# Performance work log

Hardware: AMD Instinct MI355X
Metric: run time of the kernel (lower is better)

Reference implementation:

```python
import jax, jax.numpy as jnp
import numpy as np
from jax import lax

SOS_TOKEN = 2  # prev_output initialized to [[2]] in the original module


def setup_inputs() -> dict:
    key = jax.random.key(0)
    ks = jax.random.split(key, 8)
    V, E, H, S = 32000, 512, 1024, 128
    return {
        "encoder_hn": jax.random.normal(ks[0], (1, 1, H), jnp.float32),
        "encoder_cn": jax.random.normal(ks[1], (1, 1, H), jnp.float32),
        "encoder_hidden_states": jax.random.normal(ks[2], (S, H), jnp.float32),
        "emb": jax.random.normal(ks[3], (V, E), jnp.float32) * 0.02,
        "W_ih": jax.random.normal(ks[4], (4 * H, E), jnp.float32) * 0.05,
        "W_hh": jax.random.normal(ks[5], (4 * H, H), jnp.float32) * 0.05,
        "b_ih": jnp.zeros((4 * H,), jnp.float32),
        "b_hh": jnp.zeros((4 * H,), jnp.float32),
        "W_fc": jax.random.normal(ks[6], (V, 2 * H), jnp.float32) * 0.02,
        "b_fc": jnp.zeros((V,), jnp.float32),
        "cutoff": 100,
    }


def reference(encoder_hn, encoder_cn, encoder_hidden_states, emb,
              W_ih, W_hh, b_ih, b_hh, W_fc, b_fc, cutoff):
    # Greedy sequential decode: embed -> LSTM cell -> dot attention -> concat -> fc -> log_softmax
    enc = encoder_hidden_states  # (S, H)

    def step(carry, _):
        tok, h, c = carry                       # tok: int scalar, h/c: (H,)
        x = emb[tok]                            # (E,) embedding lookup
        gates = W_ih @ x + b_ih + W_hh @ h + b_hh   # (4H,) torch LSTM gate order i,f,g,o
        i, f, g, o = jnp.split(gates, 4)
        i = jax.nn.sigmoid(i)
        f = jax.nn.sigmoid(f)
        g = jnp.tanh(g)
        o = jax.nn.sigmoid(o)
        c2 = f * c + i * g
        h2 = o * jnp.tanh(c2)
        # dot attention over encoder states
        scores = jax.nn.softmax(enc @ h2)       # (S,) softmax over seq dim
        ctx = scores @ enc                      # (H,) == enc.T @ scores
        concat = jnp.concatenate([h2, ctx])     # (2H,)
        logp = jax.nn.log_softmax(W_fc @ concat + b_fc)  # (V,)
        tok2 = jnp.argmax(logp)
        return (tok2, h2, c2), (logp, tok2)

    init = (jnp.asarray(SOS_TOKEN, jnp.int32), encoder_hn[0, 0], encoder_cn[0, 0])
    _, (preds, indices) = lax.scan(step, init, xs=None, length=int(cutoff))
    return preds, indices  # (cutoff, V), (cutoff,)
```

## Files before the change

kernel.cpp:

```cpp
#include <hip/hip_runtime.h>
#include <hip/hip_bf16.h>
#include <math.h>

#define V 32000
#define E 512
#define H 1024
#define SQ 128
#define T 100
#define NB 256
#define NTI 256
#define NTA 512
#define NTB 512
#define GROWS 16
#define FROWS 125
#define NEG_BIG (-1e30f)

typedef unsigned int u32;
typedef unsigned long long u64;

struct WS {
  float gates[4*H];
  float h[H];
  float c[2][H];
  float logits[V];
  float pmax[NB];
  float psum[NB];
  u64   pkey[NB];
};

__device__ __forceinline__ float wave_sum(float v){
  #pragma unroll
  for (int m = 32; m; m >>= 1) v += __shfl_xor(v, m, 64);
  return v;
}

__device__ __forceinline__ float wave_max(float v){
  #pragma unroll
  for (int m = 32; m; m >>= 1) v = fmaxf(v, __shfl_xor(v, m, 64));
  return v;
}

__device__ __forceinline__ u64 wave_max_u64(u64 v){
  #pragma unroll
  for (int m = 32; m; m >>= 1){
    u64 o = __shfl_xor(v, m, 64);
    v = (o > v) ? o : v;
  }
  return v;
}

__device__ __forceinline__ float dot4(float4 w, const float* v){
  return w.x*v[0] + w.y*v[1] + w.z*v[2] + w.w*v[3];
}

__global__ void __launch_bounds__(NTI) k_init(const float* __restrict__ hn,
                                              const float* __restrict__ cn,
                                              WS* __restrict__ ws){
  int tid = threadIdx.x;
  for (int j = tid; j < H; j += NTI){
    ws->h[j]    = hn[j];
    ws->c[0][j] = cn[j];
  }
  ws->pmax[tid] = NEG_BIG;
  ws->psum[tid] = 0.f;
  ws->pkey[tid] = 0ull;
}

__global__ void __launch_bounds__(NTA) k_a(const float* __restrict__ emb,
                                           const float* __restrict__ W_ih,
                                           const float* __restrict__ W_hh,
                                           const float* __restrict__ b_ih,
                                           const float* __restrict__ b_hh,
                                           WS* __restrict__ ws,
                                           float* __restrict__ out,
                                           int t){
  __shared__ float bc_logZ;
  __shared__ int   bc_tok;
  int b = blockIdx.x, tid = threadIdx.x;
  int wv = tid >> 6, ln = tid & 63;
  int tok = 2;

  if (t > 0){
    if (wv == 0){
      float mb0 = ws->pmax[ln],       mb1 = ws->pmax[ln+64];
      float mb2 = ws->pmax[ln+128],   mb3 = ws->pmax[ln+192];
      float sb0 = ws->psum[ln],       sb1 = ws->psum[ln+64];
      float sb2 = ws->psum[ln+128],   sb3 = ws->psum[ln+192];
      u64   kb0 = ws->pkey[ln],       kb1 = ws->pkey[ln+64];
      u64   kb2 = ws->pkey[ln+128],   kb3 = ws->pkey[ln+192];
      float m = wave_max(fmaxf(fmaxf(mb0, mb1), fmaxf(mb2, mb3)));
      float S = sb0*expf(mb0 - m) + sb1*expf(mb1 - m)
              + sb2*expf(mb2 - m) + sb3*expf(mb3 - m);
      S = wave_sum(S);
      u64 ka = (kb0 > kb1) ? kb0 : kb1;
      u64 kc = (kb2 > kb3) ? kb2 : kb3;
      u64 key = wave_max_u64((ka > kc) ? ka : kc);
      if (ln == 0){
        bc_logZ = m + logf(fmaxf(S, 1e-30f));
        int tk = (int)(~(u32)key);
        if ((u32)tk >= (u32)V) tk = 2;
        bc_tok = tk;
      }
    }
    __syncthreads();
    float logZ = bc_logZ;
    tok = bc_tok;

    if (tid < FROWS){
      int row = b*FROWS + tid;
      out[(size_t)(t-1)*V + row] = ws->logits[row] - logZ;
    }
    if (b == 0 && tid == 0)
      out[(size_t)T*V + (t-1)] = (float)tok;
  }

  if (t < T){
    float xv[8], hv[16];
    {
      const float4* xp = (const float4*)(emb + (size_t)tok*E) + ln*2;
      float4 x0 = xp[0], x1 = xp[1];
      xv[0]=x0.x; xv[1]=x0.y; xv[2]=x0.z; xv[3]=x0.w;
      xv[4]=x1.x; xv[5]=x1.y; xv[6]=x1.z; xv[7]=x1.w;
      const float4* hp = (const float4*)(ws->h) + ln*4;
      float4 h0 = hp[0], h1 = hp[1], h2 = hp[2], h3 = hp[3];
      hv[0]=h0.x; hv[1]=h0.y; hv[2]=h0.z; hv[3]=h0.w;
      hv[4]=h1.x; hv[5]=h1.y; hv[6]=h1.z; hv[7]=h1.w;
      hv[8]=h2.x; hv[9]=h2.y; hv[10]=h2.z; hv[11]=h2.w;
      hv[12]=h3.x; hv[13]=h3.y; hv[14]=h3.z; hv[15]=h3.w;
    }
    int rl0 = wv*2;
    int row0 = b*GROWS + rl0, row1 = row0 + 1;
    const float4* ap0 = (const float4*)(W_ih + (size_t)row0*E) + ln*2;
    const float4* ap1 = (const float4*)(W_ih + (size_t)row1*E) + ln*2;
    const float4* wh0 = (const float4*)(W_hh + (size_t)row0*H) + ln*4;
    const float4* wh1 = (const float4*)(W_hh + (size_t)row1*H) + ln*4;
    float4 ia[2], ib[2], ha[4], hb[4];
    #pragma unroll
    for (int k = 0; k < 2; ++k) ia[k] = ap0[k];
    #pragma unroll
    for (int k = 0; k < 2; ++k) ib[k] = ap1[k];
    #pragma unroll
    for (int k = 0; k < 4; ++k) ha[k] = wh0[k];
    #pragma unroll
    for (int k = 0; k < 4; ++k) hb[k] = wh1[k];
    float acc0 = dot4(ia[0], xv) + dot4(ia[1], xv+4)
               + dot4(ha[0], hv) + dot4(ha[1], hv+4) + dot4(ha[2], hv+8) + dot4(ha[3], hv+12);
    float acc1 = dot4(ib[0], xv) + dot4(ib[1], xv+4)
               + dot4(hb[0], hv) + dot4(hb[1], hv+4) + dot4(hb[2], hv+8) + dot4(hb[3], hv+12);
    acc0 = wave_sum(acc0);
    acc1 = wave_sum(acc1);
    if (ln == 0){
      ws->gates[row0] = acc0 + b_ih[row0] + b_hh[row0];
      ws->gates[row1] = acc1 + b_ih[row1] + b_hh[row1];
    }
  }
}

__global__ void __launch_bounds__(NTB) k_b(const float* __restrict__ enc,
                                           const float* __restrict__ W_fc,
                                           const float* __restrict__ b_fc,
                                           WS* __restrict__ ws,
                                           int t){
  __shared__ float concat[2*H];
  __shared__ float sc[SQ];
  __shared__ float pw[SQ];
  __shared__ float lg[128];
  int b = blockIdx.x, tid = threadIdx.x;
  int wv = tid >> 6, ln = tid & 63;

  {
    float c2v[2], h2v[2];
    #pragma unroll
    for (int k = 0; k < 2; ++k){
      int j = tid + k*NTB;
      float gi = ws->gates[j];
      float gf = ws->gates[H + j];
      float gg = ws->gates[2*H + j];
      float go = ws->gates[3*H + j];
      float co = ws->c[t & 1][j];
      float si = 1.f/(1.f + expf(-gi));
      float sf = 1.f/(1.f + expf(-gf));
      float tg = tanhf(gg);
      float so = 1.f/(1.f + expf(-go));
      float cn = sf*co + si*tg;
      float hn = so*tanhf(cn);
      c2v[k] = cn; h2v[k] = hn;
      concat[j] = hn;
    }
    if (b == 0){
      #pragma unroll
      for (int k = 0; k < 2; ++k){
        int j = tid + k*NTB;
        ws->c[(t+1) & 1][j] = c2v[k];
        ws->h[j] = h2v[k];
      }
    }
  }
  __syncthreads();

  {
    float hv[16];
    #pragma unroll
    for (int k = 0; k < 16; ++k) hv[k] = concat[ln*16 + k];
    #pragma unroll
    for (int u = 0; u < 8; ++u){
      int s0 = wv*16 + u*2, s1 = s0 + 1;
      const float4* e0p = (const float4*)(enc + (size_t)s0*H) + ln*4;
      const float4* e1p = (const float4*)(enc + (size_t)s1*H) + ln*4;
      float4 e0[4], e1[4];
      #pragma unroll
      for (int k = 0; k < 4; ++k) e0[k] = e0p[k];
      #pragma unroll
      for (int k = 0; k < 4; ++k) e1[k] = e1p[k];
      float acc0 = dot4(e0[0], hv) + dot4(e0[1], hv+4) + dot4(e0[2], hv+8) + dot4(e0[3], hv+12);
      float acc1 = dot4(e1[0], hv) + dot4(e1[1], hv+4) + dot4(e1[2], hv+8) + dot4(e1[3], hv+12);
      acc0 = wave_sum(acc0);
      acc1 = wave_sum(acc1);
      if (ln == 0){ sc[s0] = acc0; sc[s1] = acc1; }
    }
  }
  __syncthreads();

  if (wv == 0){
    float v0 = sc[ln], v1 = sc[ln + 64];
    float m = wave_max(fmaxf(v0, v1));
    float e0 = expf(v0 - m), e1 = expf(v1 - m);
    float S = wave_sum(e0 + e1);
    pw[ln]      = e0 / S;
    pw[ln + 64] = e1 / S;
  }
  __syncthreads();

  {
    float a0 = 0.f, a1 = 0.f;
    const float2* eb = (const float2*)enc + tid;
    #pragma unroll 8
    for (int s = 0; s < SQ; ++s){
      float2 e = eb[(size_t)s*(H/2)];
      float w = pw[s];
      a0 += w*e.x; a1 += w*e.y;
    }
    concat[H + tid*2 + 0] = a0;
    concat[H + tid*2 + 1] = a1;
  }
  __syncthreads();

  {
    float cv[32];
    #pragma unroll
    for (int k = 0; k < 8; ++k)
      #pragma unroll
      for (int m = 0; m < 4; ++m)
        cv[k*4 + m] = concat[k*256 + ln*4 + m];

    #pragma unroll
    for (int it = 0; it < 4; ++it){
      int l = wv*4 + it*32;
      int c0 = l,     c1 = l+1, c2 = l+2, c3 = l+3;
      if (c1 > FROWS-1) c1 = FROWS-1;
      if (c2 > FROWS-1) c2 = FROWS-1;
      if (c3 > FROWS-1) c3 = FROWS-1;
      const float4* p0 = (const float4*)(W_fc + (size_t)(b*FROWS + c0)*2048) + ln;
      const float4* p1 = (const float4*)(W_fc + (size_t)(b*FROWS + c1)*2048) + ln;
      const float4* p2 = (const float4*)(W_fc + (size_t)(b*FROWS + c2)*2048) + ln;
      const float4* p3 = (const float4*)(W_fc + (size_t)(b*FROWS + c3)*2048) + ln;
      float4 w0[8], w1[8], w2[8], w3[8];
      #pragma unroll
      for (int k = 0; k < 8; ++k) w0[k] = p0[(size_t)k*64];
      #pragma unroll
      for (int k = 0; k < 8; ++k) w1[k] = p1[(size_t)k*64];
      #pragma unroll
      for (int k = 0; k < 8; ++k) w2[k] = p2[(size_t)k*64];
      #pragma unroll
      for (int k = 0; k < 8; ++k) w3[k] = p3[(size_t)k*64];
      float a0 = 0.f, a1 = 0.f, a2 = 0.f, a3 = 0.f;
      #pragma unroll
      for (int k = 0; k < 8; ++k){
        a0 += dot4(w0[k], cv + k*4);
        a1 += dot4(w1[k], cv + k*4);
        a2 += dot4(w2[k], cv + k*4);
        a3 += dot4(w3[k], cv + k*4);
      }
      a0 = wave_sum(a0);
      a1 = wave_sum(a1);
      a2 = wave_sum(a2);
      a3 = wave_sum(a3);
      if (ln == 0){
        int row = b*FROWS + l;
        {            float x = a0 + b_fc[row];     ws->logits[row]   = x; lg[l]   = x; }
        if (l+1 < FROWS){ float x = a1 + b_fc[row+1]; ws->logits[row+1] = x; lg[l+1] = x; }
        if (l+2 < FROWS){ float x = a2 + b_fc[row+2]; ws->logits[row+2] = x; lg[l+2] = x; }
        if (l+3 < FROWS){ float x = a3 + b_fc[row+3]; ws->logits[row+3] = x; lg[l+3] = x; }
      }
    }
  }
  __syncthreads();

  if (wv == 0){
    float v0 = (ln < FROWS)      ? lg[ln]      : NEG_BIG;
    float v1 = (ln + 64 < FROWS) ? lg[ln + 64] : NEG_BIG;
    float mb = wave_max(fmaxf(v0, v1));
    float e  = expf(v0 - mb) + expf(v1 - mb);
    float sb = wave_sum(e);

    u64 k0 = 0ull, k1 = 0ull;
    if (ln < FROWS){
      u32 u = __float_as_uint(v0);
      u32 srt = (u >> 31) ? ~u : (u | 0x80000000u);
      k0 = ((u64)srt << 32) | (u32)(~(u32)(b*FROWS + ln));
    }
    if (ln + 64 < FROWS){
      u32 u = __float_as_uint(v1);
      u32 srt = (u >> 31) ? ~u : (u | 0x80000000u);
      k1 = ((u64)srt << 32) | (u32)(~(u32)(b*FROWS + ln + 64));
    }
    u64 key = wave_max_u64((k0 > k1) ? k0 : k1);

    if (ln == 0){
      ws->pmax[b] = mb;
      ws->psum[b] = sb;
      ws->pkey[b] = key;
    }
  }
}

extern "C" void kernel_launch(void* const* d_in, const int* in_sizes, int n_in,
                              void* d_out, int out_size, void* d_ws, size_t ws_size,
                              hipStream_t stream){
  const float* hn   = (const float*)d_in[0];
  const float* cn   = (const float*)d_in[1];
  const float* enc  = (const float*)d_in[2];
  const float* emb  = (const float*)d_in[3];
  const float* W_ih = (const float*)d_in[4];
  const float* W_hh = (const float*)d_in[5];
  const float* b_ih = (const float*)d_in[6];
  const float* b_hh = (const float*)d_in[7];
  const float* W_fc = (const float*)d_in[8];
  const float* b_fc = (const float*)d_in[9];
  float* out = (float*)d_out;
  WS* ws = (WS*)d_ws;
  if (ws_size < sizeof(WS)) return;

  k_init<<<1, NTI, 0, stream>>>(hn, cn, ws);
  for (int t = 0; t <= T; ++t){
    k_a<<<NB, NTA, 0, stream>>>(emb, W_ih, W_hh, b_ih, b_hh, ws, out, t);
    if (t < T) k_b<<<NB, NTB, 0, stream>>>(enc, W_fc, b_fc, ws, t);
  }
}
```

Baseline: 6.899 ms.

## Split attention into single-block kernel, removing redundant per-block attention in FC

```diff
diff --git a/kernel.cpp b/kernel.cpp
--- a/kernel.cpp
+++ b/kernel.cpp
@@ -10,7 +10,11 @@
 #define NB 256
 #define NTI 256
 #define NTA 512
-#define NTB 512
+#define NBB 500
+#define BROWS 64
+#define NTB 256
+#define NTC 1024
+#define NP 512
 #define GROWS 16
 #define FROWS 125
 #define NEG_BIG (-1e30f)
@@ -22,10 +26,11 @@
   float gates[4*H];
   float h[H];
   float c[2][H];
+  float concat[2*H];
   float logits[V];
-  float pmax[NB];
-  float psum[NB];
-  u64   pkey[NB];
+  float pmax[NP];
+  float psum[NP];
+  u64   pkey[NP];
 };
 
 __device__ __forceinline__ float wave_sum(float v){
@@ -61,9 +66,11 @@
     ws->h[j]    = hn[j];
     ws->c[0][j] = cn[j];
   }
-  ws->pmax[tid] = NEG_BIG;
-  ws->psum[tid] = 0.f;
-  ws->pkey[tid] = 0ull;
+  for (int i = tid; i < NP; i += NTI){
+    ws->pmax[i] = NEG_BIG;
+    ws->psum[i] = 0.f;
+    ws->pkey[i] = 0ull;
+  }
 }
 
 __global__ void __launch_bounds__(NTA) k_a(const float* __restrict__ emb,
@@ -82,19 +89,25 @@
 
   if (t > 0){
     if (wv == 0){
-      float mb0 = ws->pmax[ln],       mb1 = ws->pmax[ln+64];
-      float mb2 = ws->pmax[ln+128],   mb3 = ws->pmax[ln+192];
-      float sb0 = ws->psum[ln],       sb1 = ws->psum[ln+64];
-      float sb2 = ws->psum[ln+128],   sb3 = ws->psum[ln+192];
-      u64   kb0 = ws->pkey[ln],       kb1 = ws->pkey[ln+64];
-      u64   kb2 = ws->pkey[ln+128],   kb3 = ws->pkey[ln+192];
-      float m = wave_max(fmaxf(fmaxf(mb0, mb1), fmaxf(mb2, mb3)));
-      float S = sb0*expf(mb0 - m) + sb1*expf(mb1 - m)
-              + sb2*expf(mb2 - m) + sb3*expf(mb3 - m);
+      float mb[8], sb[8]; u64 kb[8];
+      #pragma unroll
+      for (int k = 0; k < 8; ++k){
+        mb[k] = ws->pmax[ln + k*64];
+        sb[k] = ws->psum[ln + k*64];
+        kb[k] = ws->pkey[ln + k*64];
+      }
+      float mx = mb[0];
+      #pragma unroll
+      for (int k = 1; k < 8; ++k) mx = fmaxf(mx, mb[k]);
+      float m = wave_max(mx);
+      float S = 0.f;
+      #pragma unroll
+      for (int k = 0; k < 8; ++k) S += sb[k] * expf(mb[k] - m);
       S = wave_sum(S);
-      u64 ka = (kb0 > kb1) ? kb0 : kb1;
-      u64 kc = (kb2 > kb3) ? kb2 : kb3;
-      u64 key = wave_max_u64((ka > kc) ? ka : kc);
+      u64 key = kb[0];
+      #pragma unroll
+      for (int k = 1; k < 8; ++k) key = (kb[k] > key) ? kb[k] : key;
+      key = wave_max_u64(key);
       if (ln == 0){
         bc_logZ = m + logf(fmaxf(S, 1e-30f));
         int tk = (int)(~(u32)key);
@@ -108,7 +121,8 @@
 
     if (tid < FROWS){
       int row = b*FROWS + tid;
-      out[(size_t)(t-1)*V + row] = ws->logits[row] - logZ;
+      __builtin_nontemporal_store(ws->logits[row] - logZ,
+                                  &out[(size_t)(t-1)*V + row]);
     }
     if (b == 0 && tid == 0)
       out[(size_t)T*V + (t-1)] = (float)tok;
@@ -156,55 +170,42 @@
   }
 }
 
-__global__ void __launch_bounds__(NTB) k_b(const float* __restrict__ enc,
-                                           const float* __restrict__ W_fc,
-                                           const float* __restrict__ b_fc,
+__global__ void __launch_bounds__(NTC) k_c(const float* __restrict__ enc,
                                            WS* __restrict__ ws,
                                            int t){
-  __shared__ float concat[2*H];
+  __shared__ float h2s[H];
   __shared__ float sc[SQ];
   __shared__ float pw[SQ];
-  __shared__ float lg[128];
-  int b = blockIdx.x, tid = threadIdx.x;
+  int tid = threadIdx.x;
   int wv = tid >> 6, ln = tid & 63;
 
   {
-    float c2v[2], h2v[2];
-    #pragma unroll
-    for (int k = 0; k < 2; ++k){
-      int j = tid + k*NTB;
-      float gi = ws->gates[j];
-      float gf = ws->gates[H + j];
-      float gg = ws->gates[2*H + j];
-      float go = ws->gates[3*H + j];
-      float co = ws->c[t & 1][j];
-      float si = 1.f/(1.f + expf(-gi));
-      float sf = 1.f/(1.f + expf(-gf));
-      float tg = tanhf(gg);
-      float so = 1.f/(1.f + expf(-go));
-      float cn = sf*co + si*tg;
-      float hn = so*tanhf(cn);
-      c2v[k] = cn; h2v[k] = hn;
-      concat[j] = hn;
-    }
-    if (b == 0){
-      #pragma unroll
-      for (int k = 0; k < 2; ++k){
-        int j = tid + k*NTB;
-        ws->c[(t+1) & 1][j] = c2v[k];
-        ws->h[j] = h2v[k];
-      }
-    }
+    int j = tid;
+    float gi = ws->gates[j];
+    float gf = ws->gates[H + j];
+    float gg = ws->gates[2*H + j];
+    float go = ws->gates[3*H + j];
+    float co = ws->c[t & 1][j];
+    float si = 1.f/(1.f + expf(-gi));
+    float sf = 1.f/(1.f + expf(-gf));
+    float tg = tanhf(gg);
+    float so = 1.f/(1.f + expf(-go));
+    float cn = sf*co + si*tg;
+    float hn = so*tanhf(cn);
+    ws->c[(t+1) & 1][j] = cn;
+    ws->h[j] = hn;
+    ws->concat[j] = hn;
+    h2s[j] = hn;
   }
   __syncthreads();
 
   {
     float hv[16];
     #pragma unroll
-    for (int k = 0; k < 16; ++k) hv[k] = concat[ln*16 + k];
-    #pragma unroll
-    for (int u = 0; u < 8; ++u){
-      int s0 = wv*16 + u*2, s1 = s0 + 1;
+    for (int k = 0; k < 16; ++k) hv[k] = h2s[ln*16 + k];
+    #pragma unroll
+    for (int u = 0; u < 4; ++u){
+      int s0 = wv*8 + u*2, s1 = s0 + 1;
       const float4* e0p = (const float4*)(enc + (size_t)s0*H) + ln*4;
       const float4* e1p = (const float4*)(enc + (size_t)s1*H) + ln*4;
       float4 e0[4], e1[4];
@@ -232,89 +233,83 @@
   __syncthreads();
 
   {
-    float a0 = 0.f, a1 = 0.f;
-    const float2* eb = (const float2*)enc + tid;
+    int col = tid;
+    float a = 0.f;
     #pragma unroll 8
-    for (int s = 0; s < SQ; ++s){
-      float2 e = eb[(size_t)s*(H/2)];
-      float w = pw[s];
-      a0 += w*e.x; a1 += w*e.y;
-    }
-    concat[H + tid*2 + 0] = a0;
-    concat[H + tid*2 + 1] = a1;
+    for (int s = 0; s < SQ; ++s)
+      a += pw[s] * enc[(size_t)s*H + col];
+    ws->concat[H + col] = a;
+  }
+}
+
+__global__ void __launch_bounds__(NTB) k_b(const float* __restrict__ W_fc,
+                                           const float* __restrict__ b_fc,
+                                           WS* __restrict__ ws){
+  __shared__ float lg[BROWS];
+  int b = blockIdx.x, tid = threadIdx.x;
+  int wv = tid >> 6, ln = tid & 63;
+
+  float cv[32];
+  {
+    const float4* cp = (const float4*)ws->concat + ln;
+    #pragma unroll
+    for (int k = 0; k < 8; ++k){
+      float4 v = cp[k*64];
+      cv[k*4+0] = v.x; cv[k*4+1] = v.y; cv[k*4+2] = v.z; cv[k*4+3] = v.w;
+    }
+  }
+
+  #pragma unroll
+  for (int it = 0; it < 4; ++it){
+    int l = wv*4 + it*16;
+    int row = b*BROWS + l;
+    const float4* p0 = (const float4*)(W_fc + (size_t)(row+0)*2048) + ln;
+    const float4* p1 = (const float4*)(W_fc + (size_t)(row+1)*2048) + ln;
+    const float4* p2 = (const float4*)(W_fc + (size_t)(row+2)*2048) + ln;
+    const float4* p3 = (const float4*)(W_fc + (size_t)(row+3)*2048) + ln;
+    float4 w0[8], w1[8], w2[8], w3[8];
+    #pragma unroll
+    for (int k = 0; k < 8; ++k) w0[k] = p0[(size_t)k*64];
+    #pragma unroll
+    for (int k = 0; k < 8; ++k) w1[k] = p1[(size_t)k*64];
+    #pragma unroll
+    for (int k = 0; k < 8; ++k) w2[k] = p2[(size_t)k*64];
+    #pragma unroll
+    for (int k = 0; k < 8; ++k) w3[k] = p3[(size_t)k*64];
+    float a0 = 0.f, a1 = 0.f, a2 = 0.f, a3 = 0.f;
+    #pragma unroll
+    for (int k = 0; k < 8; ++k){
+      a0 += dot4(w0[k], cv + k*4);
+      a1 += dot4(w1[k], cv + k*4);
+      a2 += dot4(w2[k], cv + k*4);
+      a3 += dot4(w3[k], cv + k*4);
+    }
+    a0 = wave_sum(a0);
+    a1 = wave_sum(a1);
+    a2 = wave_sum(a2);
+    a3 = wave_sum(a3);
+    if (ln == 0){
+      float x0 = a0 + b_fc[row+0];
+      float x1 = a1 + b_fc[row+1];
+      float x2 = a2 + b_fc[row+2];
+      float x3 = a3 + b_fc[row+3];
+      ws->logits[row+0] = x0; lg[l+0] = x0;
+      ws->logits[row+1] = x1; lg[l+1] = x1;
+      ws->logits[row+2] = x2; lg[l+2] = x2;
+      ws->logits[row+3] = x3; lg[l+3] = x3;
+    }
   }
   __syncthreads();
 
-  {
-    float cv[32];
-    #pragma unroll
-    for (int k = 0; k < 8; ++k)
-      #pragma unroll
-      for (int m = 0; m < 4; ++m)
-        cv[k*4 + m] = concat[k*256 + ln*4 + m];
-
-    #pragma unroll
-    for (int it = 0; it < 4; ++it){
-      int l = wv*4 + it*32;
-      int c0 = l,     c1 = l+1, c2 = l+2, c3 = l+3;
-      if (c1 > FROWS-1) c1 = FROWS-1;
-      if (c2 > FROWS-1) c2 = FROWS-1;
-      if (c3 > FROWS-1) c3 = FROWS-1;
-      const float4* p0 = (const float4*)(W_fc + (size_t)(b*FROWS + c0)*2048) + ln;
-      const float4* p1 = (const float4*)(W_fc + (size_t)(b*FROWS + c1)*2048) + ln;
-      const float4* p2 = (const float4*)(W_fc + (size_t)(b*FROWS + c2)*2048) + ln;
-      const float4* p3 = (const float4*)(W_fc + (size_t)(b*FROWS + c3)*2048) + ln;
-      float4 w0[8], w1[8], w2[8], w3[8];
-      #pragma unroll
-      for (int k = 0; k < 8; ++k) w0[k] = p0[(size_t)k*64];
-      #pragma unroll
-      for (int k = 0; k < 8; ++k) w1[k] = p1[(size_t)k*64];
-      #pragma unroll
-      for (int k = 0; k < 8; ++k) w2[k] = p2[(size_t)k*64];
-      #pragma unroll
-      for (int k = 0; k < 8; ++k) w3[k] = p3[(size_t)k*64];
-      float a0 = 0.f, a1 = 0.f, a2 = 0.f, a3 = 0.f;
-      #pragma unroll
-      for (int k = 0; k < 8; ++k){
-        a0 += dot4(w0[k], cv + k*4);
-        a1 += dot4(w1[k], cv + k*4);
-        a2 += dot4(w2[k], cv + k*4);
-        a3 += dot4(w3[k], cv + k*4);
-      }
-      a0 = wave_sum(a0);
-      a1 = wave_sum(a1);
-      a2 = wave_sum(a2);
-      a3 = wave_sum(a3);
-      if (ln == 0){
-        int row = b*FROWS + l;
-        {            float x = a0 + b_fc[row];     ws->logits[row]   = x; lg[l]   = x; }
-        if (l+1 < FROWS){ float x = a1 + b_fc[row+1]; ws->logits[row+1] = x; lg[l+1] = x; }
-        if (l+2 < FROWS){ float x = a2 + b_fc[row+2]; ws->logits[row+2] = x; lg[l+2] = x; }
-        if (l+3 < FROWS){ float x = a3 + b_fc[row+3]; ws->logits[row+3] = x; lg[l+3] = x; }
-      }
-    }
-  }
-  __syncthreads();
-
   if (wv == 0){
-    float v0 = (ln < FROWS)      ? lg[ln]      : NEG_BIG;
-    float v1 = (ln + 64 < FROWS) ? lg[ln + 64] : NEG_BIG;
-    float mb = wave_max(fmaxf(v0, v1));
-    float e  = expf(v0 - mb) + expf(v1 - mb);
-    float sb = wave_sum(e);
-
-    u64 k0 = 0ull, k1 = 0ull;
-    if (ln < FROWS){
-      u32 u = __float_as_uint(v0);
-      u32 srt = (u >> 31) ? ~u : (u | 0x80000000u);
-      k0 = ((u64)srt << 32) | (u32)(~(u32)(b*FROWS + ln));
-    }
-    if (ln + 64 < FROWS){
-      u32 u = __float_as_uint(v1);
-      u32 srt = (u >> 31) ? ~u : (u | 0x80000000u);
-      k1 = ((u64)srt << 32) | (u32)(~(u32)(b*FROWS + ln + 64));
-    }
-    u64 key = wave_max_u64((k0 > k1) ? k0 : k1);
+    float v = lg[ln];
+    float mb = wave_max(v);
+    float sb = wave_sum(expf(v - mb));
+
+    u32 u = __float_as_uint(v);
+    u32 srt = (u >> 31) ? ~u : (u | 0x80000000u);
+    u64 key = ((u64)srt << 32) | (u32)(~(u32)(b*BROWS + ln));
+    key = wave_max_u64(key);
 
     if (ln == 0){
       ws->pmax[b] = mb;
@@ -344,6 +339,9 @@
   k_init<<<1, NTI, 0, stream>>>(hn, cn, ws);
   for (int t = 0; t <= T; ++t){
     k_a<<<NB, NTA, 0, stream>>>(emb, W_ih, W_hh, b_ih, b_hh, ws, out, t);
-    if (t < T) k_b<<<NB, NTB, 0, stream>>>(enc, W_fc, b_fc, ws, t);
-  }
-}
+    if (t < T){
+      k_c<<<1,   NTC, 0, stream>>>(enc, ws, t);
+      k_b<<<NBB, NTB, 0, stream>>>(W_fc, b_fc, ws);
+    }
+  }
+}
```

New measurement: 7.578 ms. +9.8%, slower.

## Fuse decode loop into one persistent kernel with software grid barriers

Applied to the files above, without the earlier changes.

```diff
diff --git a/kernel.cpp b/kernel.cpp
--- a/kernel.cpp
+++ b/kernel.cpp
@@ -8,9 +8,11 @@
 #define SQ 128
 #define T 100
 #define NB 256
+#define NBLK 256
 #define NTI 256
 #define NTA 512
 #define NTB 512
+#define NT 512
 #define GROWS 16
 #define FROWS 125
 #define NEG_BIG (-1e30f)
@@ -26,6 +28,9 @@
   float pmax[NB];
   float psum[NB];
   u64   pkey[NB];
+  u32   pad[30];
+  u32   bar_cnt;
+  u32   bar_gen;
 };
 
 __device__ __forceinline__ float wave_sum(float v){
@@ -51,6 +56,24 @@
 
 __device__ __forceinline__ float dot4(float4 w, const float* v){
   return w.x*v[0] + w.y*v[1] + w.z*v[2] + w.w*v[3];
+}
+
+__device__ __forceinline__ void gsync(WS* ws){
+  __builtin_amdgcn_fence(__ATOMIC_RELEASE, "agent");
+  __syncthreads();
+  if (threadIdx.x == 0){
+    u32 g = __hip_atomic_load(&ws->bar_gen, __ATOMIC_RELAXED, __HIP_MEMORY_SCOPE_AGENT);
+    u32 a = __hip_atomic_fetch_add(&ws->bar_cnt, 1u, __ATOMIC_ACQ_REL, __HIP_MEMORY_SCOPE_AGENT);
+    if (a == (u32)(NBLK - 1)){
+      __hip_atomic_store(&ws->bar_cnt, 0u, __ATOMIC_RELAXED, __HIP_MEMORY_SCOPE_AGENT);
+      __hip_atomic_fetch_add(&ws->bar_gen, 1u, __ATOMIC_RELEASE, __HIP_MEMORY_SCOPE_AGENT);
+    } else {
+      while (__hip_atomic_load(&ws->bar_gen, __ATOMIC_RELAXED, __HIP_MEMORY_SCOPE_AGENT) == g)
+        __builtin_amdgcn_s_sleep(8);
+    }
+  }
+  __syncthreads();
+  __builtin_amdgcn_fence(__ATOMIC_ACQUIRE, "agent");
 }
 
 __global__ void __launch_bounds__(NTI) k_init(const float* __restrict__ hn,
@@ -64,7 +87,253 @@
   ws->pmax[tid] = NEG_BIG;
   ws->psum[tid] = 0.f;
   ws->pkey[tid] = 0ull;
-}
+  if (tid == 0){ ws->bar_cnt = 0u; ws->bar_gen = 0u; }
+}
+
+__global__ void __launch_bounds__(NT, 2)
+k_all(const float* __restrict__ hn, const float* __restrict__ cn,
+      const float* __restrict__ enc, const float* __restrict__ emb,
+      const float* __restrict__ W_ih, const float* __restrict__ W_hh,
+      const float* __restrict__ b_ih, const float* __restrict__ b_hh,
+      const float* __restrict__ W_fc, const float* __restrict__ b_fc,
+      WS* __restrict__ ws, float* __restrict__ out)
+{
+  __shared__ float hs[H];
+  __shared__ float cs[H];
+  __shared__ float cx[H];
+  __shared__ float sc[SQ];
+  __shared__ float pw[SQ];
+  __shared__ float lg[FROWS + 3];
+  __shared__ float bc_logZ;
+  __shared__ int   bc_tok;
+
+  const int b = blockIdx.x, tid = threadIdx.x;
+  const int wv = tid >> 6, ln = tid & 63;
+
+  for (int j = tid; j < H; j += NT){ hs[j] = hn[j]; cs[j] = cn[j]; }
+  __syncthreads();
+
+  int tok = 2;
+  for (int t = 0; t < T; ++t){
+    {
+      float xv[8], hv[16];
+      const float4* xp = (const float4*)(emb + (size_t)tok*E) + ln*2;
+      float4 x0 = xp[0], x1 = xp[1];
+      xv[0]=x0.x; xv[1]=x0.y; xv[2]=x0.z; xv[3]=x0.w;
+      xv[4]=x1.x; xv[5]=x1.y; xv[6]=x1.z; xv[7]=x1.w;
+      #pragma unroll
+      for (int k = 0; k < 16; ++k) hv[k] = hs[ln*16 + k];
+
+      int row0 = b*GROWS + wv*2, row1 = row0 + 1;
+      const float4* ap0 = (const float4*)(W_ih + (size_t)row0*E) + ln*2;
+      const float4* ap1 = (const float4*)(W_ih + (size_t)row1*E) + ln*2;
+      const float4* wh0 = (const float4*)(W_hh + (size_t)row0*H) + ln*4;
+      const float4* wh1 = (const float4*)(W_hh + (size_t)row1*H) + ln*4;
+      float4 ia[2], ib[2], ha[4], hb[4];
+      #pragma unroll
+      for (int k = 0; k < 2; ++k) ia[k] = ap0[k];
+      #pragma unroll
+      for (int k = 0; k < 2; ++k) ib[k] = ap1[k];
+      #pragma unroll
+      for (int k = 0; k < 4; ++k) ha[k] = wh0[k];
+      #pragma unroll
+      for (int k = 0; k < 4; ++k) hb[k] = wh1[k];
+      float acc0 = dot4(ia[0], xv) + dot4(ia[1], xv+4)
+                 + dot4(ha[0], hv) + dot4(ha[1], hv+4) + dot4(ha[2], hv+8) + dot4(ha[3], hv+12);
+      float acc1 = dot4(ib[0], xv) + dot4(ib[1], xv+4)
+                 + dot4(hb[0], hv) + dot4(hb[1], hv+4) + dot4(hb[2], hv+8) + dot4(hb[3], hv+12);
+      acc0 = wave_sum(acc0);
+      acc1 = wave_sum(acc1);
+      if (ln == 0){
+        ws->gates[row0] = acc0 + b_ih[row0] + b_hh[row0];
+        ws->gates[row1] = acc1 + b_ih[row1] + b_hh[row1];
+      }
+    }
+    gsync(ws);
+
+    {
+      #pragma unroll
+      for (int k = 0; k < 2; ++k){
+        int j = tid + k*NT;
+        float gi = ws->gates[j];
+        float gf = ws->gates[H + j];
+        float gg = ws->gates[2*H + j];
+        float go = ws->gates[3*H + j];
+        float co = cs[j];
+        float si = 1.f/(1.f + expf(-gi));
+        float sf = 1.f/(1.f + expf(-gf));
+        float tg = tanhf(gg);
+        float so = 1.f/(1.f + expf(-go));
+        float cn_ = sf*co + si*tg;
+        float hn_ = so*tanhf(cn_);
+        cs[j] = cn_;
+        hs[j] = hn_;
+      }
+    }
+    __syncthreads();
+
+    {
+      float hv[16];
+      #pragma unroll
+      for (int k = 0; k < 16; ++k) hv[k] = hs[ln*16 + k];
+      #pragma unroll
+      for (int u = 0; u < 8; ++u){
+        int s0 = wv*16 + u*2, s1 = s0 + 1;
+        const float4* e0p = (const float4*)(enc + (size_t)s0*H) + ln*4;
+        const float4* e1p = (const float4*)(enc + (size_t)s1*H) + ln*4;
+        float4 e0[4], e1[4];
+        #pragma unroll
+        for (int k = 0; k < 4; ++k) e0[k] = e0p[k];
+        #pragma unroll
+        for (int k = 0; k < 4; ++k) e1[k] = e1p[k];
+        float acc0 = dot4(e0[0], hv) + dot4(e0[1], hv+4) + dot4(e0[2], hv+8) + dot4(e0[3], hv+12);
+        float acc1 = dot4(e1[0], hv) + dot4(e1[1], hv+4) + dot4(e1[2], hv+8) + dot4(e1[3], hv+12);
+        acc0 = wave_sum(acc0);
+        acc1 = wave_sum(acc1);
+        if (ln == 0){ sc[s0] = acc0; sc[s1] = acc1; }
+      }
+    }
+    __syncthreads();
+
+    if (wv == 0){
+      float v0 = sc[ln], v1 = sc[ln + 64];
+      float m = wave_max(fmaxf(v0, v1));
+      float e0 = expf(v0 - m), e1 = expf(v1 - m);
+      float S = wave_sum(e0 + e1);
+      pw[ln]      = e0 / S;
+      pw[ln + 64] = e1 / S;
+    }
+    __syncthreads();
+
+    {
+      float a0 = 0.f, a1 = 0.f;
+      const float2* eb = (const float2*)enc + tid;
+      #pragma unroll 8
+      for (int s = 0; s < SQ; ++s){
+        float2 e = eb[(size_t)s*(H/2)];
+        float w = pw[s];
+        a0 += w*e.x; a1 += w*e.y;
+      }
+      cx[tid*2 + 0] = a0;
+      cx[tid*2 + 1] = a1;
+    }
+    __syncthreads();
+
+    {
+      float cv[32];
+      #pragma unroll
+      for (int k = 0; k < 4; ++k)
+        #pragma unroll
+        for (int m = 0; m < 4; ++m)
+          cv[k*4 + m] = hs[k*256 + ln*4 + m];
+      #pragma unroll
+      for (int k = 0; k < 4; ++k)
+        #pragma unroll
+        for (int m = 0; m < 4; ++m)
+          cv[16 + k*4 + m] = cx[k*256 + ln*4 + m];
+
+      #pragma unroll
+      for (int it = 0; it < 4; ++it){
+        int l = wv*4 + it*32;
+        int c1 = l+1, c2 = l+2, c3 = l+3;
+        if (c1 > FROWS-1) c1 = FROWS-1;
+        if (c2 > FROWS-1) c2 = FROWS-1;
+        if (c3 > FROWS-1) c3 = FROWS-1;
+        const float4* p0 = (const float4*)(W_fc + (size_t)(b*FROWS + l )*2048) + ln;
+        const float4* p1 = (const float4*)(W_fc + (size_t)(b*FROWS + c1)*2048) + ln;
+        const float4* p2 = (const float4*)(W_fc + (size_t)(b*FROWS + c2)*2048) + ln;
+        const float4* p3 = (const float4*)(W_fc + (size_t)(b*FROWS + c3)*2048) + ln;
+        float4 w0[8], w1[8], w2[8], w3[8];
+        #pragma unroll
+        for (int k = 0; k < 8; ++k) w0[k] = p0[(size_t)k*64];
+        #pragma unroll
+        for (int k = 0; k < 8; ++k) w1[k] = p1[(size_t)k*64];
+        #pragma unroll
+        for (int k = 0; k < 8; ++k) w2[k] = p2[(size_t)k*64];
+        #pragma unroll
+        for (int k = 0; k < 8; ++k) w3[k] = p3[(size_t)k*64];
+        float a0 = 0.f, a1 = 0.f, a2 = 0.f, a3 = 0.f;
+        #pragma unroll
+        for (int k = 0; k < 8; ++k){
+          a0 += dot4(w0[k], cv + k*4);
+          a1 += dot4(w1[k], cv + k*4);
+          a2 += dot4(w2[k], cv + k*4);
+          a3 += dot4(w3[k], cv + k*4);
+        }
+        a0 = wave_sum(a0);
+        a1 = wave_sum(a1);
+        a2 = wave_sum(a2);
+        a3 = wave_sum(a3);
+        if (ln == 0){
+          int row = b*FROWS + l;
+          {                 lg[l]   = a0 + b_fc[row];   }
+          if (l+1 < FROWS){ lg[l+1] = a1 + b_fc[row+1]; }
+          if (l+2 < FROWS){ lg[l+2] = a2 + b_fc[row+2]; }
+          if (l+3 < FROWS){ lg[l+3] = a3 + b_fc[row+3]; }
+        }
+      }
+    }
+    __syncthreads();
+
+    if (wv == 0){
+      float v0 = (ln < FROWS)      ? lg[ln]      : NEG_BIG;
+      float v1 = (ln + 64 < FROWS) ? lg[ln + 64] : NEG_BIG;
+      float mb = wave_max(fmaxf(v0, v1));
+      float e  = expf(v0 - mb) + expf(v1 - mb);
+      float sb = wave_sum(e);
+
+      u64 k0 = 0ull, k1 = 0ull;
+      if (ln < FROWS){
+        u32 u = __float_as_uint(v0);
+        u32 srt = (u >> 31) ? ~u : (u | 0x80000000u);
+        k0 = ((u64)srt << 32) | (u32)(~(u32)(b*FROWS + ln));
+      }
+      if (ln + 64 < FROWS){
+        u32 u = __float_as_uint(v1);
+        u32 srt = (u >> 31) ? ~u : (u | 0x80000000u);
+        k1 = ((u64)srt << 32) | (u32)(~(u32)(b*FROWS + ln + 64));
+      }
+      u64 key = wave_max_u64((k0 > k1) ? k0 : k1);
+      if (ln == 0){
+        ws->pmax[b] = mb;
+        ws->psum[b] = sb;
+        ws->pkey[b] = key;
+      }
+    }
+    gsync(ws);
+
+    if (wv == 0){
+      float mb0 = ws->pmax[ln],       mb1 = ws->pmax[ln+64];
+      float mb2 = ws->pmax[ln+128],   mb3 = ws->pmax[ln+192];
+      float sb0 = ws->psum[ln],       sb1 = ws->psum[ln+64];
+      float sb2 = ws->psum[ln+128],   sb3 = ws->psum[ln+192];
+      u64   kb0 = ws->pkey[ln],       kb1 = ws->pkey[ln+64];
+      u64   kb2 = ws->pkey[ln+128],   kb3 = ws->pkey[ln+192];
+      float m = wave_max(fmaxf(fmaxf(mb0, mb1), fmaxf(mb2, mb3)));
+      float S = sb0*expf(mb0 - m) + sb1*expf(mb1 - m)
+              + sb2*expf(mb2 - m) + sb3*expf(mb3 - m);
+      S = wave_sum(S);
+      u64 ka = (kb0 > kb1) ? kb0 : kb1;
+      u64 kc = (kb2 > kb3) ? kb2 : kb3;
+      u64 key = wave_max_u64((ka > kc) ? ka : kc);
+      if (ln == 0){
+        bc_logZ = m + logf(fmaxf(S, 1e-30f));
+        int tk = (int)(~(u32)key);
+        if ((u32)tk >= (u32)V) tk = 2;
+        bc_tok = tk;
+      }
+    }
+    __syncthreads();
+    float logZ = bc_logZ;
+    tok = bc_tok;
+
+    for (int l = tid; l < FROWS; l += NT)
+      __builtin_nontemporal_store(lg[l] - logZ, &out[(size_t)t*V + b*FROWS + l]);
+    if (b == 0 && tid == 0)
+      out[(size_t)T*V + t] = (float)tok;
+  }
+}
+
 
 __global__ void __launch_bounds__(NTA) k_a(const float* __restrict__ emb,
                                            const float* __restrict__ W_ih,
@@ -108,7 +377,8 @@
 
     if (tid < FROWS){
       int row = b*FROWS + tid;
-      out[(size_t)(t-1)*V + row] = ws->logits[row] - logZ;
+      __builtin_nontemporal_store(ws->logits[row] - logZ,
+                                  &out[(size_t)(t-1)*V + row]);
     }
     if (b == 0 && tid == 0)
       out[(size_t)T*V + (t-1)] = (float)tok;
@@ -128,8 +398,7 @@
       hv[8]=h2.x; hv[9]=h2.y; hv[10]=h2.z; hv[11]=h2.w;
       hv[12]=h3.x; hv[13]=h3.y; hv[14]=h3.z; hv[15]=h3.w;
     }
-    int rl0 = wv*2;
-    int row0 = b*GROWS + rl0, row1 = row0 + 1;
+    int row0 = b*GROWS + wv*2, row1 = row0 + 1;
     const float4* ap0 = (const float4*)(W_ih + (size_t)row0*E) + ln*2;
     const float4* ap1 = (const float4*)(W_ih + (size_t)row1*E) + ln*2;
     const float4* wh0 = (const float4*)(W_hh + (size_t)row0*H) + ln*4;
@@ -256,11 +525,11 @@
     #pragma unroll
     for (int it = 0; it < 4; ++it){
       int l = wv*4 + it*32;
-      int c0 = l,     c1 = l+1, c2 = l+2, c3 = l+3;
+      int c1 = l+1, c2 = l+2, c3 = l+3;
       if (c1 > FROWS-1) c1 = FROWS-1;
       if (c2 > FROWS-1) c2 = FROWS-1;
       if (c3 > FROWS-1) c3 = FROWS-1;
-      const float4* p0 = (const float4*)(W_fc + (size_t)(b*FROWS + c0)*2048) + ln;
+      const float4* p0 = (const float4*)(W_fc + (size_t)(b*FROWS + l )*2048) + ln;
       const float4* p1 = (const float4*)(W_fc + (size_t)(b*FROWS + c1)*2048) + ln;
       const float4* p2 = (const float4*)(W_fc + (size_t)(b*FROWS + c2)*2048) + ln;
       const float4* p3 = (const float4*)(W_fc + (size_t)(b*FROWS + c3)*2048) + ln;
@@ -287,7 +556,7 @@
       a3 = wave_sum(a3);
       if (ln == 0){
         int row = b*FROWS + l;
-        {            float x = a0 + b_fc[row];     ws->logits[row]   = x; lg[l]   = x; }
+        {                 float x = a0 + b_fc[row];   ws->logits[row]   = x; lg[l]   = x; }
         if (l+1 < FROWS){ float x = a1 + b_fc[row+1]; ws->logits[row+1] = x; lg[l+1] = x; }
         if (l+2 < FROWS){ float x = a2 + b_fc[row+2]; ws->logits[row+2] = x; lg[l+2] = x; }
         if (l+3 < FROWS){ float x = a3 + b_fc[row+3]; ws->logits[row+3] = x; lg[l+3] = x; }
@@ -342,8 +611,17 @@
   if (ws_size < sizeof(WS)) return;
 
   k_init<<<1, NTI, 0, stream>>>(hn, cn, ws);
-  for (int t = 0; t <= T; ++t){
-    k_a<<<NB, NTA, 0, stream>>>(emb, W_ih, W_hh, b_ih, b_hh, ws, out, t);
-    if (t < T) k_b<<<NB, NTB, 0, stream>>>(enc, W_fc, b_fc, ws, t);
-  }
-}
+
+  int maxb = 0;
+  hipError_t err = hipOccupancyMaxActiveBlocksPerMultiprocessor(
+      &maxb, reinterpret_cast<const void*>(k_all), NT, 0);
+  if (err == hipSuccess && maxb >= 1){
+    k_all<<<NBLK, NT, 0, stream>>>(hn, cn, enc, emb, W_ih, W_hh,
+                                   b_ih, b_hh, W_fc, b_fc, ws, out);
+  } else {
+    for (int t = 0; t <= T; ++t){
+      k_a<<<NB, NTA, 0, stream>>>(emb, W_ih, W_hh, b_ih, b_hh, ws, out, t);
+      if (t < T) k_b<<<NB, NTB, 0, stream>>>(enc, W_fc, b_fc, ws, t);
+    }
+  }
+}
```

New measurement: 6.942 ms. About the same (+0.6%).
